# Kernel optimization log

Measured on AMD Instinct MI355X. Metric: run time of the kernel, lower is better.

## Reference

```python
import jax, jax.numpy as jnp
import numpy as np

N_NODES = 100000
N_EDGES = 1600000
N_GRAPHS = 64
IN_F, HID, OUT_F = 10, 128, 101


def setup_inputs() -> dict:
    key = jax.random.key(0)
    ks = jax.random.split(key, 12)
    x = jax.random.normal(ks[0], (N_NODES, IN_F), dtype=jnp.float32)
    edge_index = jax.random.randint(ks[1], (2, N_EDGES), 0, N_NODES, dtype=jnp.int64)
    batch = jnp.sort(jax.random.randint(ks[2], (N_NODES,), 0, N_GRAPHS, dtype=jnp.int64))
    def lin(k, fi, fo):
        s = 1.0 / np.sqrt(fi)
        return jax.random.uniform(k, (fi, fo), minval=-s, maxval=s, dtype=jnp.float32)
    W1 = lin(ks[3], IN_F, HID); b1 = jnp.zeros((HID,), jnp.float32)
    W2 = lin(ks[4], HID, HID); b2 = jnp.zeros((HID,), jnp.float32)
    W3 = lin(ks[5], HID, HID); b3 = jnp.zeros((HID,), jnp.float32)
    Wl = lin(ks[6], HID, OUT_F)
    bl = jax.random.uniform(ks[7], (OUT_F,), minval=-1/np.sqrt(HID), maxval=1/np.sqrt(HID), dtype=jnp.float32)
    return {"x": x, "edge_index": edge_index, "batch": batch,
            "W1": W1, "b1": b1, "W2": W2, "b2": b2, "W3": W3, "b3": b3,
            "Wl": Wl, "bl": bl}


def _gcn_norm(edge_index, n_nodes):
    # Add self-loops and compute symmetric normalization (PyG gcn_norm).
    loop = jnp.arange(n_nodes, dtype=edge_index.dtype)
    src = jnp.concatenate([edge_index[0], loop])
    dst = jnp.concatenate([edge_index[1], loop])
    deg = jax.ops.segment_sum(jnp.ones_like(dst, dtype=jnp.float32), dst, num_segments=n_nodes)
    dis = jnp.where(deg > 0, jax.lax.rsqrt(deg), 0.0)
    w = dis[src] * dis[dst]  # [E + N]
    return src, dst, w


def _gcn_conv(x, W, b, src, dst, w, n_nodes):
    h = x @ W                      # transform first (matches GCNConv)
    msg = h[src] * w[:, None]      # gather + edge normalize
    out = jax.ops.segment_sum(msg, dst, num_segments=n_nodes)  # scatter-add
    return out + b


def reference(x, edge_index, batch, W1, b1, W2, b2, W3, b3, Wl, bl):
    n = x.shape[0]
    src, dst, w = _gcn_norm(edge_index, n)
    h = jax.nn.relu(_gcn_conv(x, W1, b1, src, dst, w, n))
    h = jax.nn.relu(_gcn_conv(h, W2, b2, src, dst, w, n))
    h = _gcn_conv(h, W3, b3, src, dst, w, n)
    # global mean pool per graph
    sums = jax.ops.segment_sum(h, batch, num_segments=N_GRAPHS)
    cnts = jax.ops.segment_sum(jnp.ones((n,), jnp.float32), batch, num_segments=N_GRAPHS)
    pooled = sums / jnp.maximum(cnts, 1.0)[:, None]
    # dropout is identity in eval mode
    return pooled @ Wl + bl
```

## Files before the change

### kernel.cpp

```cpp
#include <hip/hip_runtime.h>
#include <hip/hip_bf16.h>

#define HID 128
#define OUTF 101
#define INF 10
#define XPAD 16

#define BUCK_SHIFT 8
#define NBUCK_MAX 512
#define BCAP 4608
#define BS_TPB 256
#define BS_EPT 32
#define BS_EPB (BS_TPB * BS_EPT)

typedef __hip_bfloat16 bf16;
typedef __attribute__((ext_vector_type(8))) short short8;
typedef __attribute__((ext_vector_type(4))) float f32x4;

__device__ __forceinline__ float bflo(unsigned u) { return __uint_as_float(u << 16); }
__device__ __forceinline__ float bfhi(unsigned u) { return __uint_as_float(u & 0xffff0000u); }
__device__ __forceinline__ unsigned pk2(float a, float b) {
    __hip_bfloat162 t;
    t.x = __float2bfloat16(a);
    t.y = __float2bfloat16(b);
    return *reinterpret_cast<unsigned*>(&t);
}


__global__ void xpad_kernel(const float* __restrict__ x, float* __restrict__ xp, int n) {
    int t = blockIdx.x * blockDim.x + threadIdx.x;
    if (t >= n * XPAD) return;
    int i = t >> 4;
    int f = t & 15;
    xp[t] = (f < INF) ? x[(size_t)i * INF + f] : 0.f;
}


__global__ void init_gcur_kernel(int* __restrict__ gcur, int nbuck) {
    int b = blockIdx.x * blockDim.x + threadIdx.x;
    if (b < nbuck) gcur[b] = b * BCAP;
}

__global__ __launch_bounds__(BS_TPB) void bucket_scatter_kernel(
        const int* __restrict__ src, const int* __restrict__ dst, int E,
        int* __restrict__ gcur, int2* __restrict__ estage, int nbuck) {
    __shared__ int cnt[NBUCK_MAX];
    __shared__ int base[NBUCK_MAX];
    int tid = threadIdx.x;
    for (int b = tid; b < NBUCK_MAX; b += BS_TPB) cnt[b] = 0;
    __syncthreads();
    int e0 = blockIdx.x * BS_EPB + tid;
#pragma unroll 4
    for (int t = 0; t < BS_EPT; ++t) {
        int e = e0 + t * BS_TPB;
        if (e < E) atomicAdd(&cnt[dst[e] >> BUCK_SHIFT], 1);
    }
    __syncthreads();
    for (int b = tid; b < nbuck; b += BS_TPB) {
        int c = cnt[b];
        base[b] = c ? atomicAdd(&gcur[b], c) : 0;
    }
    __syncthreads();
    for (int b = tid; b < NBUCK_MAX; b += BS_TPB) cnt[b] = 0;
    __syncthreads();
#pragma unroll 4
    for (int t = 0; t < BS_EPT; ++t) {
        int e = e0 + t * BS_TPB;
        if (e < E) {
            int s = src[e];
            int d = dst[e];
            int bk = d >> BUCK_SHIFT;
            int o = atomicAdd(&cnt[bk], 1);
            estage[base[bk] + o] = make_int2(s, d);
        }
    }
}

__global__ __launch_bounds__(NBUCK_MAX) void scanb_kernel(const int* __restrict__ gcur,
                                                          int* __restrict__ bbase,
                                                          int* __restrict__ rowp,
                                                          int nbuck, int N) {
    __shared__ int sh[NBUCK_MAX];
    int t = threadIdx.x;
    sh[t] = (t < nbuck) ? (gcur[t] - t * BCAP) : 0;
    __syncthreads();
    for (int off = 1; off < NBUCK_MAX; off <<= 1) {
        int v = (t >= off) ? sh[t - off] : 0;
        __syncthreads();
        sh[t] += v;
        __syncthreads();
    }
    if (t < nbuck) bbase[t] = (t == 0) ? 0 : sh[t - 1];
    if (t == 0) {
        bbase[nbuck] = sh[nbuck - 1];
        rowp[N] = sh[nbuck - 1];
    }
}

__global__ __launch_bounds__(BS_TPB) void fine_scatter_kernel(
        const int2* __restrict__ estage, const int* __restrict__ bbase,
        float* __restrict__ dis, int* __restrict__ rowp,
        int* __restrict__ csrs, int n) {
    __shared__ int hist[256];
    __shared__ int pfx[256];
    __shared__ int lcur[256];
    int b = blockIdx.x;
    int tid = threadIdx.x;
    int node_lo = b << BUCK_SHIFT;
    int bb = bbase[b];
    int cnt = bbase[b + 1] - bb;
    int slo = b * BCAP;
    hist[tid] = 0;
    __syncthreads();
    for (int k = tid; k < cnt; k += BS_TPB) {
        int2 ed = estage[slo + k];
        atomicAdd(&hist[ed.y & 255], 1);
    }
    __syncthreads();
    int deg = hist[tid];
    int node = node_lo + tid;
    if (node < n) dis[node] = rsqrtf((float)(deg + 1));
    pfx[tid] = deg;
    __syncthreads();
    for (int off = 1; off < 256; off <<= 1) {
        int v = (tid >= off) ? pfx[tid - off] : 0;
        __syncthreads();
        pfx[tid] += v;
        __syncthreads();
    }
    int excl = (tid == 0) ? 0 : pfx[tid - 1];
    if (node < n) rowp[node] = bb + excl;
    lcur[tid] = excl;
    __syncthreads();
    for (int k = tid; k < cnt; k += BS_TPB) {
        int2 ed = estage[slo + k];
        int pos = bb + atomicAdd(&lcur[ed.y & 255], 1);
        csrs[pos] = ed.x;
    }
}


__global__ void agg10_kernel(const float* __restrict__ xp, const int* __restrict__ rowp,
                             const int* __restrict__ csrs, const float* __restrict__ dis,
                             float* __restrict__ ax, int n) {
    int t = threadIdx.x;
    int i = blockIdx.x * 8 + (t >> 4);
    int f = t & 15;
    if (i >= n) return;
    float dd = dis[i];
    float acc = xp[(size_t)i * XPAD + f] * dd;
    int beg = rowp[i];
    int end = rowp[i + 1];
    for (int e = beg; e < end; e += 4) {
#pragma unroll
        for (int u = 0; u < 4; ++u) {
            int ee = e + u;
            int idx = (ee < end) ? ee : end - 1;
            int s = csrs[idx];
            float w = (ee < end) ? dis[s] : 0.f;
            acc += xp[(size_t)s * XPAD + f] * w;
        }
    }
    acc *= dd;
    if (f < INF) ax[(size_t)i * INF + f] = acc;
}

__global__ void lin10_kernel(const float* __restrict__ ax, const float* __restrict__ W,
                             const float* __restrict__ b, bf16* __restrict__ h, int n) {
    int i = blockIdx.x;
    int j = threadIdx.x;
    __shared__ float xs[INF];
    if (j < INF) xs[j] = ax[(size_t)i * INF + j];
    __syncthreads();
    float acc = b[j];
#pragma unroll
    for (int k = 0; k < INF; ++k) acc += xs[k] * W[k * HID + j];
    h[(size_t)i * HID + j] = __float2bfloat16(fmaxf(acc, 0.f));
}


__global__ void wsplit_kernel(const float* __restrict__ W, bf16* __restrict__ wfh,
                              bf16* __restrict__ wfl) {
    int t = blockIdx.x * 256 + threadIdx.x;
    if (t >= HID * HID) return;
    int j    = t & 7;
    int lane = (t >> 3) & 63;
    int nt   = (t >> 9) & 7;
    int kb   = t >> 12;
    int k  = kb * 32 + (lane >> 4) * 8 + j;
    int nn = nt * 16 + (lane & 15);
    float w = W[k * HID + nn];
    float hi = __bfloat162float(__float2bfloat16(w));
    wfh[t] = __float2bfloat16(hi);
    wfl[t] = __float2bfloat16(w - hi);
}

__global__ __launch_bounds__(256) void lin128_mfma_kernel(
        const bf16* __restrict__ in, const bf16* __restrict__ wfh,
        const bf16* __restrict__ wfl, bf16* __restrict__ out, int n) {
    __shared__ short8 wh[2048];
    __shared__ short8 wl[2048];
    for (int v = threadIdx.x; v < 2048; v += 256) {
        wh[v] = ((const short8*)wfh)[v];
        wl[v] = ((const short8*)wfl)[v];
    }
    __syncthreads();

    int lane = threadIdx.x & 63;
    int wave = threadIdx.x >> 6;
    int col = lane & 15;
    int quad = lane >> 4;
    int m0 = blockIdx.x * 128 + wave * 32;

    f32x4 acc[2][8];
#pragma unroll
    for (int mt = 0; mt < 2; ++mt)
#pragma unroll
        for (int nt = 0; nt < 8; ++nt) acc[mt][nt] = (f32x4){0.f, 0.f, 0.f, 0.f};

    long rmax = n - 1;
    long r0 = m0 + col;        if (r0 > rmax) r0 = rmax;
    long r1 = m0 + 16 + col;   if (r1 > rmax) r1 = rmax;

#pragma unroll
    for (int kb = 0; kb < 4; ++kb) {
        int kofs = kb * 32 + quad * 8;
        short8 a0 = *(const short8*)(in + r0 * HID + kofs);
        short8 a1 = *(const short8*)(in + r1 * HID + kofs);
        int bbase = kb * 512 + lane;
#pragma unroll
        for (int nt = 0; nt < 8; ++nt) {
            short8 bh = wh[bbase + nt * 64];
            short8 bl = wl[bbase + nt * 64];
            acc[0][nt] = __builtin_amdgcn_mfma_f32_16x16x32_bf16(a0, bh, acc[0][nt], 0, 0, 0);
            acc[1][nt] = __builtin_amdgcn_mfma_f32_16x16x32_bf16(a1, bh, acc[1][nt], 0, 0, 0);
            acc[0][nt] = __builtin_amdgcn_mfma_f32_16x16x32_bf16(a0, bl, acc[0][nt], 0, 0, 0);
            acc[1][nt] = __builtin_amdgcn_mfma_f32_16x16x32_bf16(a1, bl, acc[1][nt], 0, 0, 0);
        }
    }

#pragma unroll
    for (int mt = 0; mt < 2; ++mt) {
        int mb = m0 + mt * 16 + quad * 4;
#pragma unroll
        for (int r = 0; r < 4; ++r) {
            int m = mb + r;
            if (m < n) {
                bf16* orow = out + (size_t)m * HID + col;
#pragma unroll
                for (int nt = 0; nt < 8; ++nt)
                    orow[nt * 16] = __float2bfloat16(acc[mt][nt][r]);
            }
        }
    }
}

__global__ __launch_bounds__(256) void agg128_kernel(
        const bf16* __restrict__ h, const int* __restrict__ rowp,
        const int* __restrict__ csrs, const float* __restrict__ dis,
        const float* __restrict__ b, bf16* __restrict__ out, int n, int relu) {
    int i = blockIdx.x * 4 + (threadIdx.x >> 6);
    if (i >= n) return;
    int lane = threadIdx.x & 63;
    int slot = lane >> 4;
    int f = lane & 15;
    float dd = dis[i];

    float acc[8];
    if (slot == 0) {
        uint4 v = *(const uint4*)(h + (size_t)i * HID + f * 8);
        acc[0] = bflo(v.x) * dd; acc[1] = bfhi(v.x) * dd;
        acc[2] = bflo(v.y) * dd; acc[3] = bfhi(v.y) * dd;
        acc[4] = bflo(v.z) * dd; acc[5] = bfhi(v.z) * dd;
        acc[6] = bflo(v.w) * dd; acc[7] = bfhi(v.w) * dd;
    } else {
#pragma unroll
        for (int j = 0; j < 8; ++j) acc[j] = 0.f;
    }

    int beg = rowp[i];
    int end = rowp[i + 1];
    for (int base = beg; base < end; base += 8) {
        int e0 = base + slot;
        int e1 = base + 4 + slot;
        int i0 = (e0 < end) ? e0 : end - 1;
        int i1 = (e1 < end) ? e1 : end - 1;
        int s0 = csrs[i0];
        int s1 = csrs[i1];
        float w0 = (e0 < end) ? dis[s0] : 0.f;
        float w1 = (e1 < end) ? dis[s1] : 0.f;
        uint4 v0 = *(const uint4*)(h + (size_t)s0 * HID + f * 8);
        uint4 v1 = *(const uint4*)(h + (size_t)s1 * HID + f * 8);
        acc[0] = fmaf(bflo(v0.x), w0, acc[0]); acc[1] = fmaf(bfhi(v0.x), w0, acc[1]);
        acc[2] = fmaf(bflo(v0.y), w0, acc[2]); acc[3] = fmaf(bfhi(v0.y), w0, acc[3]);
        acc[4] = fmaf(bflo(v0.z), w0, acc[4]); acc[5] = fmaf(bfhi(v0.z), w0, acc[5]);
        acc[6] = fmaf(bflo(v0.w), w0, acc[6]); acc[7] = fmaf(bfhi(v0.w), w0, acc[7]);
        acc[0] = fmaf(bflo(v1.x), w1, acc[0]); acc[1] = fmaf(bfhi(v1.x), w1, acc[1]);
        acc[2] = fmaf(bflo(v1.y), w1, acc[2]); acc[3] = fmaf(bfhi(v1.y), w1, acc[3]);
        acc[4] = fmaf(bflo(v1.z), w1, acc[4]); acc[5] = fmaf(bfhi(v1.z), w1, acc[5]);
        acc[6] = fmaf(bflo(v1.w), w1, acc[6]); acc[7] = fmaf(bfhi(v1.w), w1, acc[7]);
    }

#pragma unroll
    for (int j = 0; j < 8; ++j) {
        acc[j] += __shfl_xor(acc[j], 16, 64);
        acc[j] += __shfl_xor(acc[j], 32, 64);
    }

    float4 b0 = *(const float4*)(b + f * 8);
    float4 b1 = *(const float4*)(b + f * 8 + 4);
    float r[8];
    r[0] = fmaf(acc[0], dd, b0.x); r[1] = fmaf(acc[1], dd, b0.y);
    r[2] = fmaf(acc[2], dd, b0.z); r[3] = fmaf(acc[3], dd, b0.w);
    r[4] = fmaf(acc[4], dd, b1.x); r[5] = fmaf(acc[5], dd, b1.y);
    r[6] = fmaf(acc[6], dd, b1.z); r[7] = fmaf(acc[7], dd, b1.w);
    if (relu) {
#pragma unroll
        for (int j = 0; j < 8; ++j) r[j] = fmaxf(r[j], 0.f);
    }
    if (slot == 0) {
        uint4 pk;
        pk.x = pk2(r[0], r[1]);
        pk.y = pk2(r[2], r[3]);
        pk.z = pk2(r[4], r[5]);
        pk.w = pk2(r[6], r[7]);
        *(uint4*)(out + (size_t)i * HID + f * 8) = pk;
    }
}


__global__ void pool_kernel(const bf16* __restrict__ h, const int* __restrict__ batch, int n,
                            float* __restrict__ sums) {
    int g = blockIdx.x;
    int j = threadIdx.x;
    int lo = 0, hi = n;
    while (lo < hi) { int mid = (lo + hi) >> 1; if (batch[mid] < g) lo = mid + 1; else hi = mid; }
    int start = lo;
    lo = start; hi = n;
    while (lo < hi) { int mid = (lo + hi) >> 1; if (batch[mid] < g + 1) lo = mid + 1; else hi = mid; }
    int end = lo;
    float acc = 0.f;
    for (int i = start + blockIdx.y; i < end; i += gridDim.y)
        acc += __bfloat162float(h[(size_t)i * HID + j]);
    atomicAdd(&sums[g * HID + j], acc);
}

__global__ void final_kernel(const float* __restrict__ sums, const int* __restrict__ batch, int n,
                             const float* __restrict__ Wl, const float* __restrict__ bl,
                             float* __restrict__ out) {
    int g = blockIdx.x;
    int o = threadIdx.x;
    __shared__ float p[HID];
    int lo = 0, hi = n;
    while (lo < hi) { int mid = (lo + hi) >> 1; if (batch[mid] < g) lo = mid + 1; else hi = mid; }
    int start = lo;
    lo = start; hi = n;
    while (lo < hi) { int mid = (lo + hi) >> 1; if (batch[mid] < g + 1) lo = mid + 1; else hi = mid; }
    float cnt = fmaxf((float)(lo - start), 1.0f);
    p[o] = sums[g * HID + o] / cnt;
    __syncthreads();
    if (o < OUTF) {
        float acc = bl[o];
#pragma unroll 8
        for (int k = 0; k < HID; ++k) acc += p[k] * Wl[k * OUTF + o];
        out[g * OUTF + o] = acc;
    }
}


extern "C" void kernel_launch(void* const* d_in, const int* in_sizes, int n_in,
                              void* d_out, int out_size, void* d_ws, size_t ws_size,
                              hipStream_t stream) {
    const float* x   = (const float*)d_in[0];
    const int*   ei  = (const int*)d_in[1];
    const int*   bat = (const int*)d_in[2];
    const float* W1  = (const float*)d_in[3];
    const float* b1  = (const float*)d_in[4];
    const float* W2  = (const float*)d_in[5];
    const float* b2  = (const float*)d_in[6];
    const float* W3  = (const float*)d_in[7];
    const float* b3  = (const float*)d_in[8];
    const float* Wl  = (const float*)d_in[9];
    const float* bl  = (const float*)d_in[10];

    const int N = in_sizes[0] / INF;
    const int E = in_sizes[1] / 2;
    const int G = out_size / OUTF;
    const int* src = ei;
    const int* dst = ei + E;

    const int nbuck = (N + (1 << BUCK_SHIFT) - 1) >> BUCK_SHIFT;

    char* w = (char*)d_ws;
    bf16*  bufA   = (bf16*)w;  w += (size_t)N * HID * 2;
    bf16*  bufB   = (bf16*)w;  w += (size_t)N * HID * 2;
    float* ax     = (float*)w; w += (size_t)N * INF * 4;
    float* dis    = (float*)w; w += (size_t)N * 4;
    int*   rowp   = (int*)w;   w += (size_t)(N + 8) * 4;
    int*   csrs   = (int*)w;   w += (size_t)E * 4;
    float* sums   = (float*)w; w += (size_t)G * HID * 4;
    int*   gcur   = (int*)w;   w += (size_t)(nbuck + 8) * 4;
    int*   bbase  = (int*)w;   w += (size_t)(nbuck + 8) * 4;
    bf16*  wf2h   = (bf16*)w;  w += (size_t)HID * HID * 2;
    bf16*  wf2l   = (bf16*)w;  w += (size_t)HID * HID * 2;
    bf16*  wf3h   = (bf16*)w;  w += (size_t)HID * HID * 2;
    bf16*  wf3l   = (bf16*)w;  w += (size_t)HID * HID * 2;
    int2*  estage = (int2*)bufA;
    float* xp     = (float*)bufB;

    xpad_kernel<<<(N * XPAD + 255) / 256, 256, 0, stream>>>(x, xp, N);
    wsplit_kernel<<<(HID * HID + 255) / 256, 256, 0, stream>>>(W2, wf2h, wf2l);
    wsplit_kernel<<<(HID * HID + 255) / 256, 256, 0, stream>>>(W3, wf3h, wf3l);

    init_gcur_kernel<<<(nbuck + 255) / 256, 256, 0, stream>>>(gcur, nbuck);
    bucket_scatter_kernel<<<(E + BS_EPB - 1) / BS_EPB, BS_TPB, 0, stream>>>(src, dst, E, gcur,
                                                                            estage, nbuck);
    scanb_kernel<<<1, NBUCK_MAX, 0, stream>>>(gcur, bbase, rowp, nbuck, N);
    fine_scatter_kernel<<<nbuck, BS_TPB, 0, stream>>>(estage, bbase, dis, rowp, csrs, N);

    agg10_kernel<<<(N + 7) / 8, 128, 0, stream>>>(xp, rowp, csrs, dis, ax, N);
    lin10_kernel<<<N, HID, 0, stream>>>(ax, W1, b1, bufA, N);
    lin128_mfma_kernel<<<(N + 127) / 128, 256, 0, stream>>>(bufA, wf2h, wf2l, bufB, N);
    agg128_kernel<<<(N + 3) / 4, 256, 0, stream>>>(bufB, rowp, csrs, dis, b2, bufA, N, 1);
    lin128_mfma_kernel<<<(N + 127) / 128, 256, 0, stream>>>(bufA, wf3h, wf3l, bufB, N);
    agg128_kernel<<<(N + 3) / 4, 256, 0, stream>>>(bufB, rowp, csrs, dis, b3, bufA, N, 0);

    hipMemsetAsync(sums, 0, (size_t)G * HID * 4, stream);
    pool_kernel<<<dim3(G, 32), HID, 0, stream>>>(bufA, bat, N, sums);
    final_kernel<<<G, HID, 0, stream>>>(sums, bat, N, Wl, bl, (float*)d_out);
}
```

Before: 397.6 us.

## Fuse prep kernels, register-stage edges in scatters, fuse layer-1 aggregate and transform

Four small setup kernels and the memset are merged into one prep_kernel dispatched by block index, which removes several launches. Both bucket scatter kernels now load their edges into registers once instead of reading global memory in two passes. Layer-1 aggregation and the 10-to-128 linear layer are fused into one kernel: each wave splits a node's edges across four slots, reduces them with shuffles, and applies W1 in registers, so the ax intermediate buffer disappears. Risks include higher register pressure from the fixed 18-edge arrays and a silent correctness limit, since fine_scatter now assumes each bucket holds at most 18*256 edges.

Result: faster. 387.7 us (-2.5%).

```diff
diff --git a/kernel.cpp b/kernel.cpp
--- a/kernel.cpp
+++ b/kernel.cpp
@@ -9,6 +9,7 @@
 #define BUCK_SHIFT 8
 #define NBUCK_MAX 512
 #define BCAP 4608
+#define FS_EPT 18
 #define BS_TPB 256
 #define BS_EPT 32
 #define BS_EPB (BS_TPB * BS_EPT)
@@ -27,19 +28,55 @@
 }
 
 
-__global__ void xpad_kernel(const float* __restrict__ x, float* __restrict__ xp, int n) {
-    int t = blockIdx.x * blockDim.x + threadIdx.x;
-    if (t >= n * XPAD) return;
-    int i = t >> 4;
-    int f = t & 15;
-    xp[t] = (f < INF) ? x[(size_t)i * INF + f] : 0.f;
-}
-
-
-__global__ void init_gcur_kernel(int* __restrict__ gcur, int nbuck) {
-    int b = blockIdx.x * blockDim.x + threadIdx.x;
-    if (b < nbuck) gcur[b] = b * BCAP;
-}
+__device__ __forceinline__ void wsplit_body(const float* __restrict__ W, bf16* __restrict__ wfh,
+                                            bf16* __restrict__ wfl, int t) {
+    int j    = t & 7;
+    int lane = (t >> 3) & 63;
+    int nt   = (t >> 9) & 7;
+    int kb   = t >> 12;
+    int k  = kb * 32 + (lane >> 4) * 8 + j;
+    int nn = nt * 16 + (lane & 15);
+    float w = W[k * HID + nn];
+    float hi = __bfloat162float(__float2bfloat16(w));
+    wfh[t] = __float2bfloat16(hi);
+    wfl[t] = __float2bfloat16(w - hi);
+}
+
+__global__ void prep_kernel(const float* __restrict__ x, float* __restrict__ xp, int n,
+                            const float* __restrict__ W2, bf16* __restrict__ wf2h,
+                            bf16* __restrict__ wf2l,
+                            const float* __restrict__ W3, bf16* __restrict__ wf3h,
+                            bf16* __restrict__ wf3l,
+                            int* __restrict__ gcur, int nbuck,
+                            float* __restrict__ sums, int sums_n,
+                            int nb_xpad) {
+    int b = blockIdx.x;
+    int tid = threadIdx.x;
+    if (b < nb_xpad) {
+        int t = b * 256 + tid;
+        if (t < n * XPAD) {
+            int i = t >> 4;
+            int f = t & 15;
+            xp[t] = (f < INF) ? x[(size_t)i * INF + f] : 0.f;
+        }
+        return;
+    }
+    b -= nb_xpad;
+    if (b < 64) { wsplit_body(W2, wf2h, wf2l, b * 256 + tid); return; }
+    b -= 64;
+    if (b < 64) { wsplit_body(W3, wf3h, wf3l, b * 256 + tid); return; }
+    b -= 64;
+    if (b == 0) {
+        for (int k = tid; k < nbuck; k += 256) gcur[k] = k * BCAP;
+        return;
+    }
+    b -= 1;
+    {
+        int t = b * 256 + tid;
+        if (t * 4 < sums_n) ((float4*)sums)[t] = make_float4(0.f, 0.f, 0.f, 0.f);
+    }
+}
+
 
 __global__ __launch_bounds__(BS_TPB) void bucket_scatter_kernel(
         const int* __restrict__ src, const int* __restrict__ dst, int E,
@@ -47,14 +84,19 @@
     __shared__ int cnt[NBUCK_MAX];
     __shared__ int base[NBUCK_MAX];
     int tid = threadIdx.x;
-    for (int b = tid; b < NBUCK_MAX; b += BS_TPB) cnt[b] = 0;
-    __syncthreads();
     int e0 = blockIdx.x * BS_EPB + tid;
-#pragma unroll 4
+    int ds[BS_EPT], ss[BS_EPT];
+#pragma unroll
     for (int t = 0; t < BS_EPT; ++t) {
         int e = e0 + t * BS_TPB;
-        if (e < E) atomicAdd(&cnt[dst[e] >> BUCK_SHIFT], 1);
-    }
+        ds[t] = (e < E) ? dst[e] : -1;
+        ss[t] = (e < E) ? src[e] : 0;
+    }
+    for (int b = tid; b < NBUCK_MAX; b += BS_TPB) cnt[b] = 0;
+    __syncthreads();
+#pragma unroll
+    for (int t = 0; t < BS_EPT; ++t)
+        if (ds[t] >= 0) atomicAdd(&cnt[ds[t] >> BUCK_SHIFT], 1);
     __syncthreads();
     for (int b = tid; b < nbuck; b += BS_TPB) {
         int c = cnt[b];
@@ -63,17 +105,13 @@
     __syncthreads();
     for (int b = tid; b < NBUCK_MAX; b += BS_TPB) cnt[b] = 0;
     __syncthreads();
-#pragma unroll 4
-    for (int t = 0; t < BS_EPT; ++t) {
-        int e = e0 + t * BS_TPB;
-        if (e < E) {
-            int s = src[e];
-            int d = dst[e];
-            int bk = d >> BUCK_SHIFT;
+#pragma unroll
+    for (int t = 0; t < BS_EPT; ++t)
+        if (ds[t] >= 0) {
+            int bk = ds[t] >> BUCK_SHIFT;
             int o = atomicAdd(&cnt[bk], 1);
-            estage[base[bk] + o] = make_int2(s, d);
+            estage[base[bk] + o] = make_int2(ss[t], ds[t]);
         }
-    }
 }
 
 __global__ __launch_bounds__(NBUCK_MAX) void scanb_kernel(const int* __restrict__ gcur,
@@ -110,12 +148,17 @@
     int bb = bbase[b];
     int cnt = bbase[b + 1] - bb;
     int slo = b * BCAP;
+    int2 regs[FS_EPT];
+#pragma unroll
+    for (int t = 0; t < FS_EPT; ++t) {
+        int k = tid + t * BS_TPB;
+        regs[t] = (k < cnt) ? estage[slo + k] : make_int2(0, -1);
+    }
     hist[tid] = 0;
     __syncthreads();
-    for (int k = tid; k < cnt; k += BS_TPB) {
-        int2 ed = estage[slo + k];
-        atomicAdd(&hist[ed.y & 255], 1);
-    }
+#pragma unroll
+    for (int t = 0; t < FS_EPT; ++t)
+        if (regs[t].y >= 0) atomicAdd(&hist[regs[t].y & 255], 1);
     __syncthreads();
     int deg = hist[tid];
     int node = node_lo + tid;
@@ -132,68 +175,58 @@
     if (node < n) rowp[node] = bb + excl;
     lcur[tid] = excl;
     __syncthreads();
-    for (int k = tid; k < cnt; k += BS_TPB) {
-        int2 ed = estage[slo + k];
-        int pos = bb + atomicAdd(&lcur[ed.y & 255], 1);
-        csrs[pos] = ed.x;
-    }
-}
-
-
-__global__ void agg10_kernel(const float* __restrict__ xp, const int* __restrict__ rowp,
-                             const int* __restrict__ csrs, const float* __restrict__ dis,
-                             float* __restrict__ ax, int n) {
-    int t = threadIdx.x;
-    int i = blockIdx.x * 8 + (t >> 4);
-    int f = t & 15;
+#pragma unroll
+    for (int t = 0; t < FS_EPT; ++t)
+        if (regs[t].y >= 0) {
+            int pos = bb + atomicAdd(&lcur[regs[t].y & 255], 1);
+            csrs[pos] = regs[t].x;
+        }
+}
+
+__global__ __launch_bounds__(256) void aggxform10_kernel(
+        const float* __restrict__ xp, const int* __restrict__ rowp,
+        const int* __restrict__ csrs, const float* __restrict__ dis,
+        const float* __restrict__ W1, const float* __restrict__ b1,
+        bf16* __restrict__ h, int n) {
+    int i = blockIdx.x * 4 + (threadIdx.x >> 6);
     if (i >= n) return;
+    int lane = threadIdx.x & 63;
+    int slot = lane >> 4;
+    int f = lane & 15;
     float dd = dis[i];
-    float acc = xp[(size_t)i * XPAD + f] * dd;
+
+    float acc = (slot == 0) ? xp[(size_t)i * XPAD + f] * dd : 0.f;
     int beg = rowp[i];
     int end = rowp[i + 1];
-    for (int e = beg; e < end; e += 4) {
-#pragma unroll
-        for (int u = 0; u < 4; ++u) {
-            int ee = e + u;
-            int idx = (ee < end) ? ee : end - 1;
-            int s = csrs[idx];
-            float w = (ee < end) ? dis[s] : 0.f;
-            acc += xp[(size_t)s * XPAD + f] * w;
-        }
-    }
+    for (int base = beg; base < end; base += 4) {
+        int e = base + slot;
+        int idx = (e < end) ? e : end - 1;
+        int s = csrs[idx];
+        float w = (e < end) ? dis[s] : 0.f;
+        acc = fmaf(xp[(size_t)s * XPAD + f], w, acc);
+    }
+    acc += __shfl_xor(acc, 16, 64);
+    acc += __shfl_xor(acc, 32, 64);
     acc *= dd;
-    if (f < INF) ax[(size_t)i * INF + f] = acc;
-}
-
-__global__ void lin10_kernel(const float* __restrict__ ax, const float* __restrict__ W,
-                             const float* __restrict__ b, bf16* __restrict__ h, int n) {
-    int i = blockIdx.x;
-    int j = threadIdx.x;
-    __shared__ float xs[INF];
-    if (j < INF) xs[j] = ax[(size_t)i * INF + j];
-    __syncthreads();
-    float acc = b[j];
-#pragma unroll
-    for (int k = 0; k < INF; ++k) acc += xs[k] * W[k * HID + j];
-    h[(size_t)i * HID + j] = __float2bfloat16(fmaxf(acc, 0.f));
-}
-
-
-__global__ void wsplit_kernel(const float* __restrict__ W, bf16* __restrict__ wfh,
-                              bf16* __restrict__ wfl) {
-    int t = blockIdx.x * 256 + threadIdx.x;
-    if (t >= HID * HID) return;
-    int j    = t & 7;
-    int lane = (t >> 3) & 63;
-    int nt   = (t >> 9) & 7;
-    int kb   = t >> 12;
-    int k  = kb * 32 + (lane >> 4) * 8 + j;
-    int nn = nt * 16 + (lane & 15);
-    float w = W[k * HID + nn];
-    float hi = __bfloat162float(__float2bfloat16(w));
-    wfh[t] = __float2bfloat16(hi);
-    wfl[t] = __float2bfloat16(w - hi);
-}
+
+    float axk[INF];
+#pragma unroll
+    for (int k = 0; k < INF; ++k) axk[k] = __shfl(acc, k, 16);
+
+    int j0 = 2 * lane;
+    float2 bb = *(const float2*)(b1 + j0);
+    float r0 = bb.x, r1 = bb.y;
+#pragma unroll
+    for (int k = 0; k < INF; ++k) {
+        float2 wv = *(const float2*)(W1 + k * HID + j0);
+        r0 = fmaf(axk[k], wv.x, r0);
+        r1 = fmaf(axk[k], wv.y, r1);
+    }
+    r0 = fmaxf(r0, 0.f);
+    r1 = fmaxf(r1, 0.f);
+    ((unsigned*)(h + (size_t)i * HID))[lane] = pk2(r0, r1);
+}
+
 
 __global__ __launch_bounds__(256) void lin128_mfma_kernel(
         const bf16* __restrict__ in, const bf16* __restrict__ wfh,
@@ -394,7 +427,6 @@
     char* w = (char*)d_ws;
     bf16*  bufA   = (bf16*)w;  w += (size_t)N * HID * 2;
     bf16*  bufB   = (bf16*)w;  w += (size_t)N * HID * 2;
-    float* ax     = (float*)w; w += (size_t)N * INF * 4;
     float* dis    = (float*)w; w += (size_t)N * 4;
     int*   rowp   = (int*)w;   w += (size_t)(N + 8) * 4;
     int*   csrs   = (int*)w;   w += (size_t)E * 4;
@@ -408,24 +440,22 @@
     int2*  estage = (int2*)bufA;
     float* xp     = (float*)bufB;
 
-    xpad_kernel<<<(N * XPAD + 255) / 256, 256, 0, stream>>>(x, xp, N);
-    wsplit_kernel<<<(HID * HID + 255) / 256, 256, 0, stream>>>(W2, wf2h, wf2l);
-    wsplit_kernel<<<(HID * HID + 255) / 256, 256, 0, stream>>>(W3, wf3h, wf3l);
-
-    init_gcur_kernel<<<(nbuck + 255) / 256, 256, 0, stream>>>(gcur, nbuck);
+    const int nb_xpad = (N * XPAD + 255) / 256;
+    const int sums_n = G * HID;
+    prep_kernel<<<nb_xpad + 64 + 64 + 1 + 8, 256, 0, stream>>>(
+        x, xp, N, W2, wf2h, wf2l, W3, wf3h, wf3l, gcur, nbuck, sums, sums_n, nb_xpad);
+
     bucket_scatter_kernel<<<(E + BS_EPB - 1) / BS_EPB, BS_TPB, 0, stream>>>(src, dst, E, gcur,
                                                                             estage, nbuck);
     scanb_kernel<<<1, NBUCK_MAX, 0, stream>>>(gcur, bbase, rowp, nbuck, N);
     fine_scatter_kernel<<<nbuck, BS_TPB, 0, stream>>>(estage, bbase, dis, rowp, csrs, N);
 
-    agg10_kernel<<<(N + 7) / 8, 128, 0, stream>>>(xp, rowp, csrs, dis, ax, N);
-    lin10_kernel<<<N, HID, 0, stream>>>(ax, W1, b1, bufA, N);
+    aggxform10_kernel<<<(N + 3) / 4, 256, 0, stream>>>(xp, rowp, csrs, dis, W1, b1, bufA, N);
     lin128_mfma_kernel<<<(N + 127) / 128, 256, 0, stream>>>(bufA, wf2h, wf2l, bufB, N);
     agg128_kernel<<<(N + 3) / 4, 256, 0, stream>>>(bufB, rowp, csrs, dis, b2, bufA, N, 1);
     lin128_mfma_kernel<<<(N + 127) / 128, 256, 0, stream>>>(bufA, wf3h, wf3l, bufB, N);
     agg128_kernel<<<(N + 3) / 4, 256, 0, stream>>>(bufB, rowp, csrs, dis, b3, bufA, N, 0);
 
-    hipMemsetAsync(sums, 0, (size_t)G * HID * 4, stream);
     pool_kernel<<<dim3(G, 32), HID, 0, stream>>>(bufA, bat, N, sums);
     final_kernel<<<G, HID, 0, stream>>>(sums, bat, N, Wl, bl, (float*)d_out);
 }
```
